# Optimization experiments

Measured on AMD Instinct MI355X. Metric: run time of the kernel, lower is better.

Reference implementation:

```python
import jax, jax.numpy as jnp
import numpy as np

B, L, C, D = 4, 128, 1024, 512

def setup_inputs() -> dict:
    key = jax.random.key(0)
    ks = jax.random.split(key, 6)
    scale = 1.0 / np.sqrt(D)
    return {
        "hidden": jax.random.normal(ks[0], (B, L, D), dtype=jnp.float32),
        "ctx": jax.random.normal(ks[1], (B, C, D), dtype=jnp.float32),
        "W": jax.random.normal(ks[2], (D, D), dtype=jnp.float32) * scale,
        "U": jax.random.normal(ks[3], (D, D), dtype=jnp.float32) * scale,
        "U_b": jax.random.normal(ks[4], (D,), dtype=jnp.float32) * scale,
        "V": jax.random.normal(ks[5], (D,), dtype=jnp.float32) * scale,
    }

def reference(hidden, ctx, W, U, U_b, V):
    # Bahdanau additive attention: softmax_j V . tanh(W h_i + U c_j + b)
    wq = jnp.einsum('bld,ed->ble', hidden, W)          # [B, L, D]
    uc = jnp.einsum('bcd,ed->bce', ctx, U) + U_b       # [B, C, D]
    s = jnp.tanh(wq[:, :, None, :] + uc[:, None, :, :])  # [B, L, C, D]
    align = jnp.einsum('blcd,d->blc', s, V)            # [B, L, C]
    return jax.nn.softmax(align, axis=-1)
```

## Files before the change

### kernel.cpp

```cpp
#include <hip/hip_runtime.h>
#include <hip/hip_bf16.h>


#define SCALE2 2.8853900817779268f

typedef _Float16 f16x8 __attribute__((ext_vector_type(8)));
typedef float f32x4 __attribute__((ext_vector_type(4)));

__global__ __launch_bounds__(256) void gemm_mfma(
    const float* __restrict__ hidden, const float* __restrict__ ctx,
    const float* __restrict__ Wmat, const float* __restrict__ Umat,
    const float* __restrict__ U_b,
    float* __restrict__ ewq_t, float* __restrict__ euc_t)
{
    __shared__ __align__(16) _Float16 Xh[2][64][40];
    __shared__ __align__(16) _Float16 Xl[2][64][40];
    __shared__ __align__(16) _Float16 Wh[2][64][40];
    __shared__ __align__(16) _Float16 Wl[2][64][40];

    const int tid  = threadIdx.x;
    const int lane = tid & 63;
    const int w    = tid >> 6;

    const float *X, *Wm, *bias;
    float* Ct;
    int m0, crow0, Mb, bshift;
    {
        int gb = blockIdx.x;
        if (gb < 64) {
            m0 = (gb & 7) * 64; crow0 = (gb >> 3) * 64;
            X = hidden; Wm = Wmat; bias = nullptr; Ct = ewq_t; Mb = 128; bshift = 7;
        } else {
            int g = gb - 64;
            m0 = (g & 7) * 64; crow0 = (g >> 3) * 64;
            X = ctx; Wm = Umat; bias = U_b; Ct = euc_t; Mb = 1024; bshift = 10;
        }
    }

    const int sr = tid >> 2;
    const int sk = (tid & 3) * 8;
    const float* xsrc = X  + (size_t)(crow0 + sr) * 512 + sk;
    const float* wsrc = Wm + (size_t)(m0    + sr) * 512 + sk;

    f32x4 acc[4];
#pragma unroll
    for (int t = 0; t < 4; ++t) acc[t] = (f32x4){0.f, 0.f, 0.f, 0.f};

    float xrA[8], wrA[8], xrB[8], wrB[8];

#define LOADRAW(xr_, wr_, chunk)                                              \
    {                                                                         \
        float4 a_ = *(const float4*)(xsrc + (chunk) * 32);                    \
        float4 b_ = *(const float4*)(xsrc + (chunk) * 32 + 4);                \
        float4 c_ = *(const float4*)(wsrc + (chunk) * 32);                    \
        float4 d_ = *(const float4*)(wsrc + (chunk) * 32 + 4);                \
        xr_[0]=a_.x; xr_[1]=a_.y; xr_[2]=a_.z; xr_[3]=a_.w;                   \
        xr_[4]=b_.x; xr_[5]=b_.y; xr_[6]=b_.z; xr_[7]=b_.w;                   \
        wr_[0]=c_.x; wr_[1]=c_.y; wr_[2]=c_.z; wr_[3]=c_.w;                   \
        wr_[4]=d_.x; wr_[5]=d_.y; wr_[6]=d_.z; wr_[7]=d_.w;                   \
    }

#define CVTWRITE(xr_, wr_, buf)                                               \
    {                                                                         \
        f16x8 xh_, xl_, wh_, wl_;                                             \
        _Pragma("unroll")                                                     \
        for (int i_ = 0; i_ < 8; ++i_) {                                      \
            xh_[i_] = (_Float16)xr_[i_];                                      \
            xl_[i_] = (_Float16)(xr_[i_] - (float)xh_[i_]);                   \
            wh_[i_] = (_Float16)wr_[i_];                                      \
            wl_[i_] = (_Float16)(wr_[i_] - (float)wh_[i_]);                   \
        }                                                                     \
        *(f16x8*)&Xh[buf][sr][sk] = xh_; *(f16x8*)&Xl[buf][sr][sk] = xl_;     \
        *(f16x8*)&Wh[buf][sr][sk] = wh_; *(f16x8*)&Wl[buf][sr][sk] = wl_;     \
    }

    const int fr = lane & 15;
    const int fk = (lane >> 4) * 8;
    const int mrow = w * 16 + fr;

#define MFMA_CHUNK(bu)                                                        \
    {                                                                         \
        const f16x8 ah = *(const f16x8*)&Wh[bu][mrow][fk];                    \
        const f16x8 al = *(const f16x8*)&Wl[bu][mrow][fk];                    \
        _Pragma("unroll")                                                     \
        for (int t = 0; t < 4; ++t) {                                         \
            const f16x8 bh = *(const f16x8*)&Xh[bu][t * 16 + fr][fk];         \
            const f16x8 bl = *(const f16x8*)&Xl[bu][t * 16 + fr][fk];         \
            acc[t] = __builtin_amdgcn_mfma_f32_16x16x32_f16(ah, bh, acc[t], 0, 0, 0); \
            acc[t] = __builtin_amdgcn_mfma_f32_16x16x32_f16(ah, bl, acc[t], 0, 0, 0); \
            acc[t] = __builtin_amdgcn_mfma_f32_16x16x32_f16(al, bh, acc[t], 0, 0, 0); \
        }                                                                     \
    }

    LOADRAW(xrA, wrA, 0);
    CVTWRITE(xrA, wrA, 0);
    LOADRAW(xrA, wrA, 1);
    __syncthreads();

#define ITER(kc, xP, wP, xQ, wQ)                                              \
    {                                                                         \
        if ((kc) + 2 < 16) LOADRAW(xQ, wQ, (kc) + 2);                         \
        MFMA_CHUNK((kc) & 1);                                                 \
        if ((kc) + 1 < 16) CVTWRITE(xP, wP, ((kc) + 1) & 1);                  \
        __syncthreads();                                                      \
    }

#pragma unroll
    for (int kc2 = 0; kc2 < 16; kc2 += 2) {
        ITER(kc2,     xrA, wrA, xrB, wrB);
        ITER(kc2 + 1, xrB, wrB, xrA, wrA);
    }
#undef ITER
#undef MFMA_CHUNK
#undef CVTWRITE
#undef LOADRAW

    const int rbase = m0 + w * 16 + (lane >> 4) * 4;
    float bl4[4] = {0.f, 0.f, 0.f, 0.f};
    if (bias) {
        float4 t = *(const float4*)&bias[rbase];
        bl4[0] = t.x; bl4[1] = t.y; bl4[2] = t.z; bl4[3] = t.w;
    }
    const int bidx = crow0 >> bshift;
    const int cl0  = crow0 & (Mb - 1);
    float* obase = Ct + ((size_t)bidx * 512 + rbase) * Mb + cl0 + fr;
#pragma unroll
    for (int r = 0; r < 4; ++r)
#pragma unroll
        for (int t = 0; t < 4; ++t)
            obase[(size_t)r * Mb + t * 16] =
                __builtin_amdgcn_exp2f(SCALE2 * (acc[t][r] + bl4[r]));
}

__global__ __launch_bounds__(256) void fused_align14(
    const float* __restrict__ ewq_t,
    const float* __restrict__ euc_t,
    const float* __restrict__ Vv,
    float* __restrict__ pout, float* __restrict__ part1)
{
    __shared__ __align__(16) float uc_s[128][128];
    __shared__ __align__(16) float wq_s[128][16];
    __shared__ __align__(16) float v_s[256];

    const int tid  = threadIdx.x;
    const int lane = tid & 63;
    const int w    = __builtin_amdgcn_readfirstlane(tid >> 6);
    const int c0   = blockIdx.x * 128;
    const int l0   = blockIdx.y * 16;
    const int z    = blockIdx.z;
    const int b    = z >> 1, h = z & 1;
    const int d0   = h * 256;

    const float* ucb = euc_t + ((size_t)b * 512 + d0) * 1024 + c0;
    const float* wqb = ewq_t + ((size_t)b * 512 + d0) * 128 + l0;

    if (tid < 64)
        *(float4*)&v_s[tid * 4] = *(const float4*)(Vv + d0 + tid * 4);

    const int urow = w * 32 + (lane >> 5);
    const int ucol = (lane & 31) * 4;
    const int qrow = tid >> 1, qcol = (tid & 1) * 8;

    float acc[4][2];
#pragma unroll
    for (int l = 0; l < 4; ++l) { acc[l][0] = 0.f; acc[l][1] = 0.f; }

    for (int ch = 0; ch < 2; ++ch) {
        __syncthreads();
        {
            const float* src = ucb + (size_t)(ch * 128) * 1024;
#pragma unroll
            for (int p = 0; p < 16; ++p)
                *(float4*)&uc_s[urow + p * 2][ucol] =
                    *(const float4*)(src + (size_t)(urow + p * 2) * 1024 + ucol);
            const float* qsrc = wqb + (size_t)(ch * 128) * 128 + (size_t)qrow * 128 + qcol;
            *(float4*)&wq_s[qrow][qcol]     = *(const float4*)(qsrc);
            *(float4*)&wq_s[qrow][qcol + 4] = *(const float4*)(qsrc + 4);
        }
        __syncthreads();

#pragma unroll 8
        for (int qd = 0; qd < 32; ++qd) {
            const int dd = qd * 4;
            const float2 e0 = *(const float2*)&uc_s[dd + 0][lane * 2];
            const float2 e1 = *(const float2*)&uc_s[dd + 1][lane * 2];
            const float2 e2 = *(const float2*)&uc_s[dd + 2][lane * 2];
            const float2 e3 = *(const float2*)&uc_s[dd + 3][lane * 2];
            const float4 q0 = *(const float4*)&wq_s[dd + 0][w * 4];
            const float4 q1 = *(const float4*)&wq_s[dd + 1][w * 4];
            const float4 q2 = *(const float4*)&wq_s[dd + 2][w * 4];
            const float4 q3 = *(const float4*)&wq_s[dd + 3][w * 4];
            const float4 vq = *(const float4*)&v_s[ch * 128 + dd];
            const float e0a[2] = {e0.x, e0.y};
            const float e1a[2] = {e1.x, e1.y};
            const float e2a[2] = {e2.x, e2.y};
            const float e3a[2] = {e3.x, e3.y};
            const float q0a[4] = {q0.x, q0.y, q0.z, q0.w};
            const float q1a[4] = {q1.x, q1.y, q1.z, q1.w};
            const float q2a[4] = {q2.x, q2.y, q2.z, q2.w};
            const float q3a[4] = {q3.x, q3.y, q3.z, q3.w};
#pragma unroll
            for (int l = 0; l < 4; ++l) {
#pragma unroll
                for (int k = 0; k < 2; ++k) {
                    const float t0 = fmaf(q0a[l], e0a[k], 1.0f);
                    const float t1 = fmaf(q1a[l], e1a[k], 1.0f);
                    const float t2 = fmaf(q2a[l], e2a[k], 1.0f);
                    const float t3 = fmaf(q3a[l], e3a[k], 1.0f);
                    const float A  = t0 * t1;
                    const float B  = t2 * t3;
                    const float n01 = fmaf(vq.x, t1, vq.y * t0);
                    const float n23 = fmaf(vq.z, t3, vq.w * t2);
                    const float N   = fmaf(n01, B, n23 * A);
                    acc[l][k] = fmaf(N, __builtin_amdgcn_rcpf(A * B), acc[l][k]);
                }
            }
        }
    }

    float* pp = h ? part1 : pout;
#pragma unroll
    for (int l = 0; l < 4; ++l) {
        float2 o;
        o.x = -2.0f * acc[l][0];
        o.y = -2.0f * acc[l][1];
        *(float2*)(pp + ((size_t)b * 128 + l0 + w * 4 + l) * 1024 + c0 + lane * 2) = o;
    }
}

__global__ __launch_bounds__(256) void softmax7(
    float* __restrict__ data, const float* __restrict__ part1)
{
    __shared__ float red[8];
    const int row  = blockIdx.x;
    const int tid  = threadIdx.x;
    const int w    = tid >> 6;
    const int lane = tid & 63;
    float* p = data + (size_t)row * 1024;

    float4 x = *(const float4*)(p + tid * 4);
    {
        const float4 a = *(const float4*)(part1 + (size_t)row * 1024 + tid * 4);
        x.x += a.x; x.y += a.y; x.z += a.z; x.w += a.w;
    }

    float m = fmaxf(fmaxf(x.x, x.y), fmaxf(x.z, x.w));
#pragma unroll
    for (int mask = 32; mask >= 1; mask >>= 1) m = fmaxf(m, __shfl_xor(m, mask, 64));
    if (lane == 0) red[w] = m;
    __syncthreads();
    m = fmaxf(fmaxf(red[0], red[1]), fmaxf(red[2], red[3]));

    const float LOG2E = 1.4426950408889634f;
    x.x = __builtin_amdgcn_exp2f((x.x - m) * LOG2E);
    x.y = __builtin_amdgcn_exp2f((x.y - m) * LOG2E);
    x.z = __builtin_amdgcn_exp2f((x.z - m) * LOG2E);
    x.w = __builtin_amdgcn_exp2f((x.w - m) * LOG2E);
    float s = (x.x + x.y) + (x.z + x.w);
#pragma unroll
    for (int mask = 32; mask >= 1; mask >>= 1) s += __shfl_xor(s, mask, 64);
    if (lane == 0) red[4 + w] = s;
    __syncthreads();
    s = (red[4] + red[5]) + (red[6] + red[7]);

    const float rr = __builtin_amdgcn_rcpf(s);
    x.x *= rr; x.y *= rr; x.z *= rr; x.w *= rr;
    *(float4*)(p + tid * 4) = x;
}

extern "C" void kernel_launch(void* const* d_in, const int* in_sizes, int n_in,
                              void* d_out, int out_size, void* d_ws, size_t ws_size,
                              hipStream_t stream)
{
    const float* hidden = (const float*)d_in[0];
    const float* ctx    = (const float*)d_in[1];
    const float* W      = (const float*)d_in[2];
    const float* U      = (const float*)d_in[3];
    const float* U_b    = (const float*)d_in[4];
    const float* V      = (const float*)d_in[5];
    float* out = (float*)d_out;

    float* ewq_t = (float*)d_ws;
    float* euc_t = ewq_t + 4 * 512 * 128;
    float* part1 = euc_t + 4 * 512 * 1024;

    gemm_mfma<<<576, 256, 0, stream>>>(hidden, ctx, W, U, U_b, ewq_t, euc_t);
    fused_align14<<<dim3(8, 8, 8), 256, 0, stream>>>(ewq_t, euc_t, V, out, part1);
    softmax7<<<512, 256, 0, stream>>>(out, part1);
}
```

Baseline: 54.95 us.

## Drop D-split partials and use pairwise reciprocal grouping in align kernel

The align kernel now processes the full 512-wide D per block, so the second partial buffer and the extra add in softmax are removed. Tiles shrink to 64 context columns with one column per lane. The tanh product trick groups two d-terms per reciprocal instead of four, which raises reciprocal count and per-term arithmetic in exchange for the saved global traffic.

```diff
diff --git a/kernel.cpp b/kernel.cpp
--- a/kernel.cpp
+++ b/kernel.cpp
@@ -132,104 +132,92 @@
                 __builtin_amdgcn_exp2f(SCALE2 * (acc[t][r] + bl4[r]));
 }
 
-__global__ __launch_bounds__(256) void fused_align14(
+__global__ __launch_bounds__(256) void fused_align17(
     const float* __restrict__ ewq_t,
     const float* __restrict__ euc_t,
     const float* __restrict__ Vv,
-    float* __restrict__ pout, float* __restrict__ part1)
-{
-    __shared__ __align__(16) float uc_s[128][128];
-    __shared__ __align__(16) float wq_s[128][16];
-    __shared__ __align__(16) float v_s[256];
+    float* __restrict__ out)
+{
+    __shared__ float uc_s[128][64];
+    __shared__ float wq_s[128][16];
+    __shared__ float v_s[512];
 
     const int tid  = threadIdx.x;
     const int lane = tid & 63;
     const int w    = __builtin_amdgcn_readfirstlane(tid >> 6);
-    const int c0   = blockIdx.x * 128;
-    const int l0   = blockIdx.y * 16;
-    const int z    = blockIdx.z;
-    const int b    = z >> 1, h = z & 1;
-    const int d0   = h * 256;
-
-    const float* ucb = euc_t + ((size_t)b * 512 + d0) * 1024 + c0;
-    const float* wqb = ewq_t + ((size_t)b * 512 + d0) * 128 + l0;
-
-    if (tid < 64)
-        *(float4*)&v_s[tid * 4] = *(const float4*)(Vv + d0 + tid * 4);
-
-    const int urow = w * 32 + (lane >> 5);
-    const int ucol = (lane & 31) * 4;
-    const int qrow = tid >> 1, qcol = (tid & 1) * 8;
-
-    float acc[4][2];
-#pragma unroll
-    for (int l = 0; l < 4; ++l) { acc[l][0] = 0.f; acc[l][1] = 0.f; }
-
-    for (int ch = 0; ch < 2; ++ch) {
+    const int c0   = blockIdx.x * 64;
+    const int lblk = blockIdx.y * 16;
+    const int b    = blockIdx.z;
+
+    const float* ucb = euc_t + (size_t)b * 512 * 1024 + c0;
+    const float* wqb = ewq_t + (size_t)b * 512 * 128 + lblk;
+
+    v_s[tid]       = Vv[tid];
+    v_s[tid + 256] = Vv[tid + 256];
+
+    float a0 = 0.f, a1 = 0.f, a2 = 0.f, a3 = 0.f;
+
+    for (int dc = 0; dc < 4; ++dc) {
         __syncthreads();
         {
-            const float* src = ucb + (size_t)(ch * 128) * 1024;
-#pragma unroll
-            for (int p = 0; p < 16; ++p)
-                *(float4*)&uc_s[urow + p * 2][ucol] =
-                    *(const float4*)(src + (size_t)(urow + p * 2) * 1024 + ucol);
-            const float* qsrc = wqb + (size_t)(ch * 128) * 128 + (size_t)qrow * 128 + qcol;
-            *(float4*)&wq_s[qrow][qcol]     = *(const float4*)(qsrc);
-            *(float4*)&wq_s[qrow][qcol + 4] = *(const float4*)(qsrc + 4);
+            const float* src = ucb + (size_t)(dc * 128) * 1024;
+            const int row = tid >> 4, col = (tid & 15) * 4;
+#pragma unroll
+            for (int p = 0; p < 8; ++p)
+                *(float4*)&uc_s[p * 16 + row][col] =
+                    *(const float4*)(src + (size_t)(p * 16 + row) * 1024 + col);
+        }
+        {
+            const float* src = wqb + (size_t)(dc * 128) * 128;
+            const int row = tid >> 1, col = (tid & 1) * 8;
+            *(float4*)&wq_s[row][col]     = *(const float4*)(src + (size_t)row * 128 + col);
+            *(float4*)&wq_s[row][col + 4] = *(const float4*)(src + (size_t)row * 128 + col + 4);
         }
         __syncthreads();
 
+        const float* vs = &v_s[dc * 128];
 #pragma unroll 8
-        for (int qd = 0; qd < 32; ++qd) {
-            const int dd = qd * 4;
-            const float2 e0 = *(const float2*)&uc_s[dd + 0][lane * 2];
-            const float2 e1 = *(const float2*)&uc_s[dd + 1][lane * 2];
-            const float2 e2 = *(const float2*)&uc_s[dd + 2][lane * 2];
-            const float2 e3 = *(const float2*)&uc_s[dd + 3][lane * 2];
-            const float4 q0 = *(const float4*)&wq_s[dd + 0][w * 4];
-            const float4 q1 = *(const float4*)&wq_s[dd + 1][w * 4];
-            const float4 q2 = *(const float4*)&wq_s[dd + 2][w * 4];
-            const float4 q3 = *(const float4*)&wq_s[dd + 3][w * 4];
-            const float4 vq = *(const float4*)&v_s[ch * 128 + dd];
-            const float e0a[2] = {e0.x, e0.y};
-            const float e1a[2] = {e1.x, e1.y};
-            const float e2a[2] = {e2.x, e2.y};
-            const float e3a[2] = {e3.x, e3.y};
-            const float q0a[4] = {q0.x, q0.y, q0.z, q0.w};
-            const float q1a[4] = {q1.x, q1.y, q1.z, q1.w};
-            const float q2a[4] = {q2.x, q2.y, q2.z, q2.w};
-            const float q3a[4] = {q3.x, q3.y, q3.z, q3.w};
-#pragma unroll
-            for (int l = 0; l < 4; ++l) {
-#pragma unroll
-                for (int k = 0; k < 2; ++k) {
-                    const float t0 = fmaf(q0a[l], e0a[k], 1.0f);
-                    const float t1 = fmaf(q1a[l], e1a[k], 1.0f);
-                    const float t2 = fmaf(q2a[l], e2a[k], 1.0f);
-                    const float t3 = fmaf(q3a[l], e3a[k], 1.0f);
-                    const float A  = t0 * t1;
-                    const float B  = t2 * t3;
-                    const float n01 = fmaf(vq.x, t1, vq.y * t0);
-                    const float n23 = fmaf(vq.z, t3, vq.w * t2);
-                    const float N   = fmaf(n01, B, n23 * A);
-                    acc[l][k] = fmaf(N, __builtin_amdgcn_rcpf(A * B), acc[l][k]);
-                }
-            }
-        }
-    }
-
-    float* pp = h ? part1 : pout;
-#pragma unroll
-    for (int l = 0; l < 4; ++l) {
-        float2 o;
-        o.x = -2.0f * acc[l][0];
-        o.y = -2.0f * acc[l][1];
-        *(float2*)(pp + ((size_t)b * 128 + l0 + w * 4 + l) * 1024 + c0 + lane * 2) = o;
-    }
-}
-
-__global__ __launch_bounds__(256) void softmax7(
-    float* __restrict__ data, const float* __restrict__ part1)
+        for (int j = 0; j < 64; ++j) {
+            const float  e0 = uc_s[2 * j][lane];
+            const float  e1 = uc_s[2 * j + 1][lane];
+            const float4 q0 = *(const float4*)&wq_s[2 * j][w * 4];
+            const float4 q1 = *(const float4*)&wq_s[2 * j + 1][w * 4];
+            const float2 v2 = *(const float2*)&vs[2 * j];
+            {
+                const float t0 = fmaf(q0.x, e0, 1.0f);
+                const float t1 = fmaf(q1.x, e1, 1.0f);
+                a0 = fmaf(fmaf(v2.x, t1, v2.y * t0),
+                          __builtin_amdgcn_rcpf(t0 * t1), a0);
+            }
+            {
+                const float t0 = fmaf(q0.y, e0, 1.0f);
+                const float t1 = fmaf(q1.y, e1, 1.0f);
+                a1 = fmaf(fmaf(v2.x, t1, v2.y * t0),
+                          __builtin_amdgcn_rcpf(t0 * t1), a1);
+            }
+            {
+                const float t0 = fmaf(q0.z, e0, 1.0f);
+                const float t1 = fmaf(q1.z, e1, 1.0f);
+                a2 = fmaf(fmaf(v2.x, t1, v2.y * t0),
+                          __builtin_amdgcn_rcpf(t0 * t1), a2);
+            }
+            {
+                const float t0 = fmaf(q0.w, e0, 1.0f);
+                const float t1 = fmaf(q1.w, e1, 1.0f);
+                a3 = fmaf(fmaf(v2.x, t1, v2.y * t0),
+                          __builtin_amdgcn_rcpf(t0 * t1), a3);
+            }
+        }
+    }
+
+    float* op = out + ((size_t)b * 128 + lblk + w * 4) * 1024 + c0 + lane;
+    op[0]    = -2.0f * a0;
+    op[1024] = -2.0f * a1;
+    op[2048] = -2.0f * a2;
+    op[3072] = -2.0f * a3;
+}
+
+__global__ __launch_bounds__(256) void softmax8(float* __restrict__ data)
 {
     __shared__ float red[8];
     const int row  = blockIdx.x;
@@ -239,10 +227,6 @@
     float* p = data + (size_t)row * 1024;
 
     float4 x = *(const float4*)(p + tid * 4);
-    {
-        const float4 a = *(const float4*)(part1 + (size_t)row * 1024 + tid * 4);
-        x.x += a.x; x.y += a.y; x.z += a.z; x.w += a.w;
-    }
 
     float m = fmaxf(fmaxf(x.x, x.y), fmaxf(x.z, x.w));
 #pragma unroll
@@ -282,9 +266,8 @@
 
     float* ewq_t = (float*)d_ws;
     float* euc_t = ewq_t + 4 * 512 * 128;
-    float* part1 = euc_t + 4 * 512 * 1024;
 
     gemm_mfma<<<576, 256, 0, stream>>>(hidden, ctx, W, U, U_b, ewq_t, euc_t);
-    fused_align14<<<dim3(8, 8, 8), 256, 0, stream>>>(ewq_t, euc_t, V, out, part1);
-    softmax7<<<512, 256, 0, stream>>>(out, part1);
-}
+    fused_align17<<<dim3(16, 8, 4), 256, 0, stream>>>(ewq_t, euc_t, V, out);
+    softmax8<<<512, 256, 0, stream>>>(out);
+}
```

New measurement: 58.06 us. 1.06x slower.
